# Kernel tuning notes

Measured on AMD Instinct MI355X. Metric: run time of the kernel, lower is better.

## Reference

```python
import jax, jax.numpy as jnp
import numpy as np
from jax import lax

B, N_PATCH, D_ENC, D, L, HEADS, NCLS = 2, 640, 512, 256, 2, 8, 3
IMG, PS, NSC = 256, 16, 2
MAX_SCALE = NSC - 1
NEW_GS = IMG // (PS // (2 ** MAX_SCALE))  # 32
STAGES = 3  # log2(IMG / NEW_GS)
HD = D // HEADS


def _make_patch_code():
    # valid multiscale partition, sorted by scale (the torch code assumes this)
    base = IMG // PS  # 16x16 scale-0 grid
    pc = []
    for c in range(base * base // 2):
        pc.append((0, c))
    for c in range(base * base // 2, base * base):
        r0, c0 = divmod(c, base)
        for a in range(2):
            for b in range(2):
                pc.append((1, (2 * r0 + a) * (2 * base) + (2 * c0 + b)))
    return np.asarray(pc, dtype=np.int64)


def setup_inputs():
    key = jax.random.key(0)
    ks = iter(jax.random.split(key, 48))
    nrm = lambda *s: jax.random.normal(next(ks), s, jnp.float32) * 0.02
    z = lambda *s: jnp.zeros(s, jnp.float32)
    o = lambda *s: jnp.ones(s, jnp.float32)
    return {
        "x": jax.random.normal(next(ks), (B, N_PATCH, D_ENC), jnp.float32),
        "patch_code": jnp.asarray(_make_patch_code()),
        "proj_dec_w": nrm(D_ENC, D), "proj_dec_b": z(D),
        "pos_w1": nrm(2, D), "pos_b1": z(D),
        "pos_w2": nrm(D, D), "pos_b2": z(D),
        "cls_emb": nrm(1, D, D),
        "ln1_g": o(L, D), "ln1_b": z(L, D),
        "qkv_w": nrm(L, D, 3 * D), "qkv_b": z(L, 3 * D),
        "attn_w": nrm(L, D, D), "attn_b": z(L, D),
        "ln2_g": o(L, D), "ln2_b": z(L, D),
        "mlp_w1": nrm(L, D, 4 * D), "mlp_b1": z(L, 4 * D),
        "mlp_w2": nrm(L, 4 * D, D), "mlp_b2": z(L, D),
        "dec_g": o(D), "dec_b": z(D),
        "proj_patch": jax.random.normal(next(ks), (D, D), jnp.float32) * D ** -0.5,
        "proj_classes": jax.random.normal(next(ks), (D, D), jnp.float32) * D ** -0.5,
        "mask_g": o(D), "mask_b": z(D),
        "up_conv_w": nrm(STAGES, D, D, 3, 3), "up_conv_b": z(STAGES, D),
        "up_convt_w": nrm(STAGES, D, D, 2, 2), "up_convt_b": z(STAGES, D),
        "out_conv_w": nrm(NCLS, D, 3, 3), "out_conv_b": z(NCLS),
    }


def _ln(x, g, b, eps=1e-5):
    m = x.mean(-1, keepdims=True)
    v = jnp.mean((x - m) ** 2, axis=-1, keepdims=True)
    return (x - m) / jnp.sqrt(v + eps) * g + b


def _inorm(x, eps=1e-5):  # InstanceNorm2d, affine=False
    m = x.mean((2, 3), keepdims=True)
    v = jnp.mean((x - m) ** 2, axis=(2, 3), keepdims=True)
    return (x - m) / jnp.sqrt(v + eps)


def _leaky(x):
    return jnp.where(x >= 0, x, 0.01 * x)


def _conv3(x, w, b):
    y = lax.conv_general_dilated(x, w, (1, 1), 'SAME', dimension_numbers=('NCHW', 'OIHW', 'NCHW'))
    return y + b[None, :, None, None]


def _convt2(x, w, b):
    # ConvTranspose2d(k=2, s=2): non-overlapping, exact as einsum + reshape
    bsz, _, h, wd = x.shape
    y = jnp.einsum('bchw,cdij->bdhiwj', x, w).reshape(bsz, w.shape[1], 2 * h, 2 * wd)
    return y + b[None, :, None, None]


def _block(x, l, ln1_g, ln1_b, qkv_w, qkv_b, attn_w, attn_b, ln2_g, ln2_b, mlp_w1, mlp_b1, mlp_w2, mlp_b2):
    bsz, s, _ = x.shape
    h = _ln(x, ln1_g[l], ln1_b[l])
    qkv = (h @ qkv_w[l] + qkv_b[l]).reshape(bsz, s, 3, HEADS, HD)
    q, k, v = qkv[:, :, 0], qkv[:, :, 1], qkv[:, :, 2]  # [b,s,h,d]
    att = jax.nn.softmax(jnp.einsum('bqhd,bkhd->bhqk', q, k) * HD ** -0.5, axis=-1)
    out = jnp.einsum('bhqk,bkhd->bqhd', att, v).reshape(bsz, s, D)
    x = x + out @ attn_w[l] + attn_b[l]
    h = _ln(x, ln2_g[l], ln2_b[l])
    x = x + jax.nn.gelu(h @ mlp_w1[l] + mlp_b1[l], approximate=False) @ mlp_w2[l] + mlp_b2[l]
    return x


def reference(x, patch_code, proj_dec_w, proj_dec_b, pos_w1, pos_b1, pos_w2, pos_b2, cls_emb, ln1_g, ln1_b, qkv_w, qkv_b, attn_w, attn_b, ln2_g, ln2_b, mlp_w1, mlp_b1, mlp_w2, mlp_b2, dec_g, dec_b, proj_patch, proj_classes, mask_g, mask_b, up_conv_w, up_conv_b, up_convt_w, up_convt_b, out_conv_w, out_conv_b):
    bsz = x.shape[0]
    x = x @ proj_dec_w + proj_dec_b
    pcf = patch_code.astype(jnp.float32)
    pos = jax.nn.relu(pcf @ pos_w1 + pos_b1) @ pos_w2 + pos_b2  # [N, D]
    x = x + pos[None]
    x = jnp.concatenate([x, jnp.broadcast_to(cls_emb, (bsz, D, D))], axis=1)  # seq = N + D
    for l in range(L):
        x = _block(x, l, ln1_g, ln1_b, qkv_w, qkv_b, attn_w, attn_b, ln2_g, ln2_b, mlp_w1, mlp_b1, mlp_w2, mlp_b2)
    x = _ln(x, dec_g, dec_b)
    patches, cls_feat = x[:, :-D], x[:, -D:]
    patches = patches @ proj_patch
    cls_feat = cls_feat @ proj_classes
    patches = patches / jnp.linalg.norm(patches, axis=-1, keepdims=True)
    cls_feat = cls_feat / jnp.linalg.norm(cls_feat, axis=-1, keepdims=True)
    masks = _ln(jnp.einsum('bnd,bkd->bnk', patches, cls_feat), mask_g, mask_b)  # [B,N,D]
    vals = masks.transpose(0, 2, 1)  # [B, C=D, N]
    # patches_to_images: scatter variable-size patches into the finest grid.
    # Implemented as an inverse map (cell -> source patch) + gather, which is
    # exact because patch_code is a partition of the image.
    s = patch_code[:, 0]
    coord = patch_code[:, 1]
    gs = (IMG // PS) * jnp.power(2, s)          # grid size at each patch's scale
    k = jnp.power(2, MAX_SCALE - s)             # footprint in finest-grid cells
    r = (coord // gs) * k
    c = (coord % gs) * k
    K = 2 ** MAX_SCALE
    oi = jnp.arange(K)[:, None]
    oj = jnp.arange(K)[None, :]
    rr = r[:, None, None] + oi[None]
    cc = c[:, None, None] + oj[None]
    valid = (oi[None] < k[:, None, None]) & (oj[None] < k[:, None, None])
    flat = jnp.where(valid, rr * NEW_GS + cc, NEW_GS * NEW_GS).reshape(-1)
    pid = jnp.broadcast_to(jnp.arange(N_PATCH)[:, None, None], (N_PATCH, K, K)).reshape(-1)
    inv = jnp.zeros(NEW_GS * NEW_GS + 1, jnp.int32).at[flat].set(pid.astype(jnp.int32))
    img = vals[:, :, inv[:NEW_GS * NEW_GS]].reshape(bsz, D, NEW_GS, NEW_GS)
    for i in range(STAGES):
        img = _leaky(_inorm(_conv3(img, up_conv_w[i], up_conv_b[i])))
        img = _leaky(_inorm(_convt2(img, up_convt_w[i], up_convt_b[i])))
    return _conv3(img, out_conv_w, out_conv_b)  # [B, n_cls, 256, 256]
```

## Files before the change

### kernel.cpp

```cpp
#include <hip/hip_runtime.h>
#include <hip/hip_bf16.h>

typedef __hip_bfloat16 bf16;
typedef _Float16 f16;
typedef __attribute__((ext_vector_type(8))) _Float16 f16x8;
typedef __attribute__((ext_vector_type(4))) float f32x4;

__global__ void detect_k(const unsigned short* __restrict__ xh, int* __restrict__ flags)
{
  const int t = threadIdx.x;
  int w = 0;
  for (int i = t; i < 512; i += 64) {
    const int e = (xh[i] >> 7) & 0xFF;
    if (e == 0xFF || e >= 0x88) ++w;
  }
  #pragma unroll
  for (int msk = 1; msk < 64; msk <<= 1) w += __shfl_xor(w, msk);
  if (t == 0) flags[0] = (w > 32) ? 1 : 0;
}

#define NSEG 33
struct CvtDesc {
  const void* src[NSEG];
  unsigned dstOff[NSEG];
  unsigned n[NSEG];
};
__global__ __launch_bounds__(256) void cvtall_k(
    CvtDesc d, float* __restrict__ P, const int* __restrict__ flags)
{
  const int s = blockIdx.y;
  const unsigned n = d.n[s];
  const int fp32 = flags[0];
  float* dst = P + d.dstOff[s];
  const unsigned stride = gridDim.x * 256u;
  if (fp32) {
    const float* src = (const float*)d.src[s];
    for (unsigned i = blockIdx.x * 256u + threadIdx.x; i < n; i += stride) dst[i] = src[i];
  } else {
    const bf16* src = (const bf16*)d.src[s];
    for (unsigned i = blockIdx.x * 256u + threadIdx.x; i < n; i += stride)
      dst[i] = __bfloat162float(src[i]);
  }
}

__global__ __launch_bounds__(256) void prepw_k(
    const float* __restrict__ ucw, const float* __restrict__ utw, const float* __restrict__ ocw,
    f16* __restrict__ wf3, f16* __restrict__ wt, f16* __restrict__ wocp)
{
  const int n1 = 3 * 9 * 65536;
  const int n2 = 3 * 4 * 65536;
  const int n3 = 9 * 16 * 256;
  for (int i = blockIdx.x * 256 + threadIdx.x; i < n1 + n2 + n3; i += gridDim.x * 256) {
    if (i < n1) {
      const int st = i / 589824, r = i % 589824;
      const int kk = r / 65536, rr = r % 65536;
      const int co = rr >> 8, ci = rr & 255;
      wf3[i] = (f16)ucw[(((size_t)st * 256 + co) * 256 + ci) * 9 + kk];
    } else if (i < n1 + n2) {
      const int j = i - n1;
      const int st = j / 262144, r = j % 262144;
      const int ij = r / 65536, rr = r % 65536;
      const int co = rr >> 8, ci = rr & 255;
      wt[j] = (f16)utw[(((size_t)st * 256 + ci) * 256 + co) * 4 + ij];
    } else {
      const int j = i - n1 - n2;
      const int tap = j >> 12, rem = j & 4095;
      const int co = rem >> 8, ci = rem & 255;
      wocp[j] = (co < 3) ? (f16)ocw[(((size_t)co * 256) + ci) * 9 + tap] : (f16)0.f;
    }
  }
}

template<bool TRB, int ACT>
__global__ __launch_bounds__(256) void gemm64_k(
    const float* __restrict__ A, const float* __restrict__ B,
    const float* __restrict__ bias, const float* __restrict__ res,
    float* __restrict__ C, int M, int N, int K)
{
  const int m0 = blockIdx.y << 6, n0 = blockIdx.x << 6;
  const int t = threadIdx.x;
  const int lane = t & 63, wv = t >> 6;
  const int wm = wv >> 1, wn = wv & 1;
  const int frow = lane & 15, kg = lane >> 4;
  __shared__ f16 As[64][40];
  __shared__ f16 Bs[64][40];
  f32x4 acc[2][2];
  #pragma unroll
  for (int i = 0; i < 2; ++i)
    #pragma unroll
    for (int j = 0; j < 2; ++j) acc[i][j] = (f32x4){0.f, 0.f, 0.f, 0.f};

  for (int k0 = 0; k0 < K; k0 += 32) {
    __syncthreads();
    {
      const int row = t >> 2, kh = (t & 3) << 3;
      const float* ap = A + (size_t)(m0 + row) * K + k0 + kh;
      #pragma unroll
      for (int j = 0; j < 8; ++j) As[row][kh + j] = (f16)ap[j];
    }
    if (TRB) {
      const int row = t >> 2, kh = (t & 3) << 3;
      const float* bp = B + (size_t)(n0 + row) * K + k0 + kh;
      #pragma unroll
      for (int j = 0; j < 8; ++j) Bs[row][kh + j] = (f16)bp[j];
    } else {
      #pragma unroll
      for (int i2 = 0; i2 < 8; ++i2) {
        const int i = i2 * 256 + t;
        const int n = i & 63, kk = i >> 6;
        Bs[n][kk] = (f16)B[(size_t)(k0 + kk) * N + n0 + n];
      }
    }
    __syncthreads();
    f16x8 af[2], bf[2];
    #pragma unroll
    for (int fm = 0; fm < 2; ++fm)
      af[fm] = *(const f16x8*)&As[wm * 32 + fm * 16 + frow][kg * 8];
    #pragma unroll
    for (int fn = 0; fn < 2; ++fn)
      bf[fn] = *(const f16x8*)&Bs[wn * 32 + fn * 16 + frow][kg * 8];
    #pragma unroll
    for (int fm = 0; fm < 2; ++fm)
      #pragma unroll
      for (int fn = 0; fn < 2; ++fn)
        acc[fm][fn] = __builtin_amdgcn_mfma_f32_16x16x32_f16(af[fm], bf[fn], acc[fm][fn], 0, 0, 0);
  }
  #pragma unroll
  for (int fn = 0; fn < 2; ++fn) {
    const int col = n0 + wn * 32 + fn * 16 + frow;
    const float bv = bias ? bias[col] : 0.f;
    #pragma unroll
    for (int fm = 0; fm < 2; ++fm)
      #pragma unroll
      for (int r = 0; r < 4; ++r) {
        const int row = m0 + wm * 32 + fm * 16 + kg * 4 + r;
        float v = acc[fm][fn][r] + bv;
        if (ACT == 1) v = 0.5f * v * (1.0f + erff(v * 0.70710678118654752f));
        if (res) v += res[(size_t)row * N + col];
        C[(size_t)row * N + col] = v;
      }
  }
}

__global__ __launch_bounds__(256) void ln_k(
    const float* __restrict__ in, float* __restrict__ out,
    const float* __restrict__ g, const float* __restrict__ b)
{
  const int row = blockIdx.x, t = threadIdx.x;
  __shared__ float ws1[4], ws2[4];
  const float x = in[(size_t)row * 256 + t];
  float v = x;
  #pragma unroll
  for (int msk = 1; msk < 64; msk <<= 1) v += __shfl_xor(v, msk);
  if ((t & 63) == 0) ws1[t >> 6] = v;
  __syncthreads();
  const float m = (ws1[0] + ws1[1] + ws1[2] + ws1[3]) * (1.0f / 256.0f);
  const float d = x - m;
  float v2 = d * d;
  #pragma unroll
  for (int msk = 1; msk < 64; msk <<= 1) v2 += __shfl_xor(v2, msk);
  if ((t & 63) == 0) ws2[t >> 6] = v2;
  __syncthreads();
  const float rstd = rsqrtf((ws2[0] + ws2[1] + ws2[2] + ws2[3]) * (1.0f / 256.0f) + 1e-5f);
  out[(size_t)row * 256 + t] = d * rstd * g[t] + b[t];
}

__global__ __launch_bounds__(256) void l2n_k(float* __restrict__ x)
{
  const int row = blockIdx.x, t = threadIdx.x;
  __shared__ float ws[4];
  const float v = x[(size_t)row * 256 + t];
  float s = v * v;
  #pragma unroll
  for (int msk = 1; msk < 64; msk <<= 1) s += __shfl_xor(s, msk);
  if ((t & 63) == 0) ws[t >> 6] = s;
  __syncthreads();
  x[(size_t)row * 256 + t] = v * rsqrtf(ws[0] + ws[1] + ws[2] + ws[3]);
}

__global__ __launch_bounds__(256) void posh_k(
    const int* __restrict__ pc, const float* __restrict__ w1, const float* __restrict__ b1,
    float* __restrict__ hid)
{
  const int n = blockIdx.x, t = threadIdx.x;
  const int wide = (pc[3] == 0);
  const int sv = wide ? pc[4 * n] : pc[2 * n];
  const int cv = wide ? pc[4 * n + 2] : pc[2 * n + 1];
  const float hv = (float)sv * w1[t] + (float)cv * w1[256 + t] + b1[t];
  hid[(size_t)n * 256 + t] = hv > 0.0f ? hv : 0.0f;
}

__global__ __launch_bounds__(256) void assemble_k(
    const float* __restrict__ proj, const float* __restrict__ pos,
    const float* __restrict__ cls, float* __restrict__ xb)
{
  const int row = blockIdx.x;
  const int b = row / 896, n = row % 896, t = threadIdx.x;
  float v;
  if (n < 640) v = proj[((size_t)b * 640 + n) * 256 + t] + pos[n * 256 + t];
  else         v = cls[(n - 640) * 256 + t];
  xb[(size_t)row * 256 + t] = v;
}

__global__ __launch_bounds__(128) void attnm_k(
    const float* __restrict__ qkv, float* __restrict__ out)
{
  const int q0 = blockIdx.x << 5;
  const int h = blockIdx.y, b = blockIdx.z;
  const int t = threadIdx.x;
  const int lane = t & 63, wv = t >> 6;
  const int c = lane & 15, kg = lane >> 4;
  __shared__ f16 Qs[32][36];
  __shared__ f16 Ks[64][36];
  __shared__ f16 Vt[32][68];
  __shared__ f16 Pl[2][16][68];
  {
    const int row = t >> 2, part = t & 3;
    const float* src = qkv + ((size_t)(b * 896 + q0 + row) * 768) + h * 32 + part * 8;
    f16 tmp[8];
    #pragma unroll
    for (int j = 0; j < 8; ++j) tmp[j] = (f16)(src[j] * 0.17677669529663687f);
    *(f16x8*)&Qs[row][part * 8] = *(const f16x8*)tmp;
  }
  const f32x4 z4 = {0.f, 0.f, 0.f, 0.f};
  f32x4 o0 = z4, o1 = z4;
  float m[4] = {-1e30f, -1e30f, -1e30f, -1e30f};
  float l[4] = {0.f, 0.f, 0.f, 0.f};

  for (int k0 = 0; k0 < 896; k0 += 64) {
    __syncthreads();
    for (int i = t; i < 256; i += 128) {
      const int row = i >> 2, part = i & 3;
      const float* src = qkv + ((size_t)(b * 896 + k0 + row) * 768) + 256 + h * 32 + part * 8;
      f16 tmp[8];
      #pragma unroll
      for (int j = 0; j < 8; ++j) tmp[j] = (f16)src[j];
      *(f16x8*)&Ks[row][part * 8] = *(const f16x8*)tmp;
    }
    for (int i = t; i < 256; i += 128) {
      const int row = i >> 2, part = i & 3;
      const float* src = qkv + ((size_t)(b * 896 + k0 + row) * 768) + 512 + h * 32 + part * 8;
      #pragma unroll
      for (int j = 0; j < 8; ++j) Vt[part * 8 + j][row] = (f16)src[j];
    }
    __syncthreads();
    const f16x8 aq = *(const f16x8*)&Qs[wv * 16 + c][kg * 8];
    f32x4 s[4];
    #pragma unroll
    for (int fn = 0; fn < 4; ++fn)
      s[fn] = __builtin_amdgcn_mfma_f32_16x16x32_f16(
          aq, *(const f16x8*)&Ks[fn * 16 + c][kg * 8], z4, 0, 0, 0);
    float sc[4];
    #pragma unroll
    for (int r = 0; r < 4; ++r) {
      float v = fmaxf(fmaxf(s[0][r], s[1][r]), fmaxf(s[2][r], s[3][r]));
      #pragma unroll
      for (int msk = 1; msk < 16; msk <<= 1) v = fmaxf(v, __shfl_xor(v, msk));
      const float mn = fmaxf(m[r], v);
      sc[r] = __expf(m[r] - mn);
      m[r] = mn;
    }
    #pragma unroll
    for (int r = 0; r < 4; ++r) {
      float ps = 0.f;
      #pragma unroll
      for (int fn = 0; fn < 4; ++fn) {
        const float p = __expf(s[fn][r] - m[r]);
        ps += p;
        Pl[wv][kg * 4 + r][fn * 16 + c] = (f16)p;
      }
      #pragma unroll
      for (int msk = 1; msk < 16; msk <<= 1) ps += __shfl_xor(ps, msk);
      l[r] = l[r] * sc[r] + ps;
    }
    #pragma unroll
    for (int r = 0; r < 4; ++r) { o0[r] *= sc[r]; o1[r] *= sc[r]; }
    const f16x8 a0 = *(const f16x8*)&Pl[wv][c][kg * 8];
    const f16x8 a1 = *(const f16x8*)&Pl[wv][c][32 + kg * 8];
    o0 = __builtin_amdgcn_mfma_f32_16x16x32_f16(a0, *(const f16x8*)&Vt[c][kg * 8], o0, 0, 0, 0);
    o0 = __builtin_amdgcn_mfma_f32_16x16x32_f16(a1, *(const f16x8*)&Vt[c][32 + kg * 8], o0, 0, 0, 0);
    o1 = __builtin_amdgcn_mfma_f32_16x16x32_f16(a0, *(const f16x8*)&Vt[16 + c][kg * 8], o1, 0, 0, 0);
    o1 = __builtin_amdgcn_mfma_f32_16x16x32_f16(a1, *(const f16x8*)&Vt[16 + c][32 + kg * 8], o1, 0, 0, 0);
  }
  #pragma unroll
  for (int r = 0; r < 4; ++r) {
    const int row = q0 + wv * 16 + kg * 4 + r;
    const float inv = 1.0f / l[r];
    out[((size_t)(b * 896 + row) * 256) + h * 32 + c] = o0[r] * inv;
    out[((size_t)(b * 896 + row) * 256) + h * 32 + 16 + c] = o1[r] * inv;
  }
}

__global__ __launch_bounds__(1024) void inv_k(const int* __restrict__ pc, int* __restrict__ inv)
{
  const int t = threadIdx.x;
  if (t < 1024) inv[t] = 0;
  __syncthreads();
  if (t < 640) {
    const int wide = (pc[3] == 0);
    int s = wide ? pc[4 * t] : pc[2 * t];
    int coord = wide ? pc[4 * t + 2] : pc[2 * t + 1];
    s &= 1;
    const int gs = 16 << s;
    const int k = 1 << (1 - s);
    const int r = (coord / gs) * k, c = (coord % gs) * k;
    for (int oi = 0; oi < k; ++oi)
      for (int oj = 0; oj < k; ++oj) {
        const int rr = r + oi, cc = c + oj;
        if (rr >= 0 && rr < 32 && cc >= 0 && cc < 32)
          inv[rr * 32 + cc] = t;
      }
  }
}

__global__ __launch_bounds__(256) void gather16_k(
    const float* __restrict__ masks, const int* __restrict__ inv, f16* __restrict__ img)
{
  const int p = blockIdx.x & 1023, b = blockIdx.x >> 10, t = threadIdx.x;
  img[((size_t)blockIdx.x << 8) + t] = (f16)masks[((size_t)b * 640 + inv[p]) * 256 + t];
}

__global__ __launch_bounds__(256) void conv3m_k(
    const f16* __restrict__ x, const f16* __restrict__ wf, const float* __restrict__ bias,
    f16* __restrict__ y, int H, int W)
{
  const int tilesx = W >> 4;
  const int ty0 = (blockIdx.x / tilesx) << 4, tx0 = (blockIdx.x % tilesx) << 4;
  const int co0 = blockIdx.y << 6;
  const int b = blockIdx.z;
  const int t = threadIdx.x;
  const int lane = t & 63, wv = t >> 6;
  const int frow = lane & 15, kg = lane >> 4;
  __shared__ f16 halo[18][18][40];
  __shared__ f16 bt9[9][64][40];
  f32x4 acc[4][4];
  #pragma unroll
  for (int i = 0; i < 4; ++i)
    #pragma unroll
    for (int j = 0; j < 4; ++j) acc[i][j] = (f32x4){0.f, 0.f, 0.f, 0.f};

  for (int c0 = 0; c0 < 256; c0 += 32) {
    __syncthreads();
    for (int i = t; i < 1296; i += 256) {
      const int cell = i >> 2, part = i & 3;
      const int hy = cell / 18, hx = cell - hy * 18;
      const int gy = ty0 + hy - 1, gx = tx0 + hx - 1;
      f16x8 v = {(f16)0,(f16)0,(f16)0,(f16)0,(f16)0,(f16)0,(f16)0,(f16)0};
      if (gy >= 0 && gy < H && gx >= 0 && gx < W)
        v = *(const f16x8*)&x[(((size_t)b * H + gy) * W + gx) * 256 + c0 + part * 8];
      *(f16x8*)&halo[hy][hx][part * 8] = v;
    }
    for (int i = t; i < 2304; i += 256) {
      const int tap = i >> 8, rem = i & 255, co = rem >> 2, part = rem & 3;
      *(f16x8*)&bt9[tap][co][part * 8] =
          *(const f16x8*)&wf[(((size_t)tap * 256) + co0 + co) * 256 + c0 + part * 8];
    }
    __syncthreads();
    #pragma unroll
    for (int kyr = 0; kyr < 3; ++kyr)
      #pragma unroll
      for (int kx = 0; kx < 3; ++kx) {
        f16x8 af[4], bf[4];
        #pragma unroll
        for (int fm = 0; fm < 4; ++fm) {
          const int pos = wv * 64 + fm * 16 + frow;
          af[fm] = *(const f16x8*)&halo[(pos >> 4) + kyr][(pos & 15) + kx][kg * 8];
        }
        #pragma unroll
        for (int fn = 0; fn < 4; ++fn)
          bf[fn] = *(const f16x8*)&bt9[kyr * 3 + kx][fn * 16 + frow][kg * 8];
        #pragma unroll
        for (int fm = 0; fm < 4; ++fm)
          #pragma unroll
          for (int fn = 0; fn < 4; ++fn)
            acc[fm][fn] = __builtin_amdgcn_mfma_f32_16x16x32_f16(af[fm], bf[fn], acc[fm][fn], 0, 0, 0);
      }
  }
  #pragma unroll
  for (int fn = 0; fn < 4; ++fn) {
    const int col = co0 + fn * 16 + frow;
    const float bv = bias[col];
    #pragma unroll
    for (int fm = 0; fm < 4; ++fm)
      #pragma unroll
      for (int r = 0; r < 4; ++r) {
        const int pos = wv * 64 + fm * 16 + kg * 4 + r;
        y[(((size_t)b * H + ty0 + (pos >> 4)) * W + tx0 + (pos & 15)) * 256 + col] =
            (f16)(acc[fm][fn][r] + bv);
      }
  }
}

__global__ __launch_bounds__(256) void convtm_k(
    const f16* __restrict__ x, const f16* __restrict__ wtp, const float* __restrict__ bias,
    f16* __restrict__ y, int H, int W)
{
  const int tilesx = W >> 4;
  const int ty0 = (blockIdx.x / tilesx) << 4, tx0 = (blockIdx.x % tilesx) << 4;
  const int co0 = (blockIdx.y >> 2) << 6;
  const int par = blockIdx.y & 3;
  const int pa = par >> 1, pb = par & 1;
  const int b = blockIdx.z;
  const int t = threadIdx.x;
  const int lane = t & 63, wv = t >> 6;
  const int frow = lane & 15, kg = lane >> 4;
  __shared__ f16 at[256][40];
  __shared__ f16 btw[64][40];
  f32x4 acc[4][4];
  #pragma unroll
  for (int i = 0; i < 4; ++i)
    #pragma unroll
    for (int j = 0; j < 4; ++j) acc[i][j] = (f32x4){0.f, 0.f, 0.f, 0.f};

  for (int c0 = 0; c0 < 256; c0 += 32) {
    __syncthreads();
    for (int i = t; i < 1024; i += 256) {
      const int cell = i >> 2, part = i & 3;
      const int gy = ty0 + (cell >> 4), gx = tx0 + (cell & 15);
      *(f16x8*)&at[cell][part * 8] =
          *(const f16x8*)&x[(((size_t)b * H + gy) * W + gx) * 256 + c0 + part * 8];
    }
    {
      const int i = t;
      const int co = i >> 2, part = i & 3;
      *(f16x8*)&btw[co][part * 8] =
          *(const f16x8*)&wtp[((size_t)par * 256 + co0 + co) * 256 + c0 + part * 8];
    }
    __syncthreads();
    f16x8 af[4], bf[4];
    #pragma unroll
    for (int fm = 0; fm < 4; ++fm)
      af[fm] = *(const f16x8*)&at[wv * 64 + fm * 16 + frow][kg * 8];
    #pragma unroll
    for (int fn = 0; fn < 4; ++fn)
      bf[fn] = *(const f16x8*)&btw[fn * 16 + frow][kg * 8];
    #pragma unroll
    for (int fm = 0; fm < 4; ++fm)
      #pragma unroll
      for (int fn = 0; fn < 4; ++fn)
        acc[fm][fn] = __builtin_amdgcn_mfma_f32_16x16x32_f16(af[fm], bf[fn], acc[fm][fn], 0, 0, 0);
  }
  const int HO = H << 1, WO = W << 1;
  #pragma unroll
  for (int fn = 0; fn < 4; ++fn) {
    const int col = co0 + fn * 16 + frow;
    const float bv = bias[col];
    #pragma unroll
    for (int fm = 0; fm < 4; ++fm)
      #pragma unroll
      for (int r = 0; r < 4; ++r) {
        const int pos = wv * 64 + fm * 16 + kg * 4 + r;
        const int oy = ((ty0 + (pos >> 4)) << 1) + pa;
        const int ox = ((tx0 + (pos & 15)) << 1) + pb;
        y[(((size_t)b * HO + oy) * WO + ox) * 256 + col] = (f16)(acc[fm][fn][r] + bv);
      }
  }
}

__global__ __launch_bounds__(256) void stats1v_k(
    const f16* __restrict__ x, float2* __restrict__ partial, int HW, int NS)
{
  const int s = blockIdx.x, b = blockIdx.y, t = threadIdx.x;
  const int rg = t >> 5, cp = t & 31;
  const int rpb = HW / NS;
  const f16* p = x + ((size_t)b * HW + (size_t)s * rpb) * 256 + cp * 8;
  float s1[8] = {}, s2[8] = {};
  for (int r = rg; r < rpb; r += 8) {
    const f16x8 v = *(const f16x8*)&p[(size_t)r * 256];
    #pragma unroll
    for (int j = 0; j < 8; ++j) { const float f = (float)v[j]; s1[j] += f; s2[j] += f * f; }
  }
  __shared__ float red[2][8][256];
  #pragma unroll
  for (int j = 0; j < 8; ++j) { red[0][rg][cp * 8 + j] = s1[j]; red[1][rg][cp * 8 + j] = s2[j]; }
  __syncthreads();
  float a1 = 0.f, a2 = 0.f;
  #pragma unroll
  for (int g = 0; g < 8; ++g) { a1 += red[0][g][t]; a2 += red[1][g][t]; }
  partial[((size_t)b * NS + s) * 256 + t] = make_float2(a1, a2);
}

__global__ __launch_bounds__(256) void stats2_k(
    const float2* __restrict__ partial, float2* __restrict__ mr, int HW)
{
  const int cg = blockIdx.x, b = blockIdx.y, t = threadIdx.x;
  const int chl = t & 31, g = t >> 5;
  const int ch = cg * 32 + chl;
  float s1 = 0.f, s2 = 0.f;
  for (int s = g * 16; s < g * 16 + 16; ++s) {
    const float2 v = partial[((size_t)b * 128 + s) * 256 + ch];
    s1 += v.x; s2 += v.y;
  }
  __shared__ float r1[8][32], r2[8][32];
  r1[g][chl] = s1; r2[g][chl] = s2;
  __syncthreads();
  if (t < 32) {
    float a1 = 0.f, a2 = 0.f;
    #pragma unroll
    for (int gg = 0; gg < 8; ++gg) { a1 += r1[gg][t]; a2 += r2[gg][t]; }
    const float m = a1 / (float)HW;
    const float var = fmaxf(a2 / (float)HW - m * m, 0.f);
    mr[b * 256 + cg * 32 + t] = make_float2(m, rsqrtf(var + 1e-5f));
  }
}

__global__ __launch_bounds__(256) void norm8_k(
    f16* __restrict__ x, const float2* __restrict__ mr, int HW)
{
  const int b = blockIdx.y, t = threadIdx.x;
  const int cp = t & 31, rg = t >> 5;
  float2 mv[8];
  {
    const float2* mrb = mr + b * 256 + cp * 8;
    #pragma unroll
    for (int j = 0; j < 8; ++j) mv[j] = mrb[j];
  }
  f16* p = x + ((size_t)b * HW + (size_t)blockIdx.x * 64) * 256 + cp * 8;
  #pragma unroll
  for (int r8 = 0; r8 < 8; ++r8) {
    const int r = rg + r8 * 8;
    f16x8 v = *(const f16x8*)&p[(size_t)r * 256];
    #pragma unroll
    for (int j = 0; j < 8; ++j) {
      const float z = ((float)v[j] - mv[j].x) * mv[j].y;
      v[j] = (f16)(z >= 0.f ? z : 0.01f * z);
    }
    *(f16x8*)&p[(size_t)r * 256] = v;
  }
}

__global__ __launch_bounds__(256) void convoutm2_k(
    const f16* __restrict__ x, const f16* __restrict__ wocp, const float* __restrict__ bias,
    void* __restrict__ yv, const int* __restrict__ flags)
{
  const int ty0 = (blockIdx.x >> 4) << 4, tx0 = (blockIdx.x & 15) << 4;
  const int b = blockIdx.y;
  const int t = threadIdx.x;
  const int lane = t & 63, wv = t >> 6;
  const int frow = lane & 15, kg = lane >> 4;
  __shared__ f16 halo[18][18][40];
  f32x4 acc[4];
  #pragma unroll
  for (int i = 0; i < 4; ++i) acc[i] = (f32x4){0.f, 0.f, 0.f, 0.f};

  for (int c0 = 0; c0 < 256; c0 += 32) {
    __syncthreads();
    for (int i = t; i < 1296; i += 256) {
      const int cell = i >> 2, part = i & 3;
      const int hy = cell / 18, hx = cell - hy * 18;
      const int gy = ty0 + hy - 1, gx = tx0 + hx - 1;
      f16x8 v = {(f16)0,(f16)0,(f16)0,(f16)0,(f16)0,(f16)0,(f16)0,(f16)0};
      if ((unsigned)gy < 256u && (unsigned)gx < 256u)
        v = *(const f16x8*)&x[(((size_t)b * 256 + gy) * 256 + gx) * 256 + c0 + part * 8];
      *(f16x8*)&halo[hy][hx][part * 8] = v;
    }
    __syncthreads();
    #pragma unroll
    for (int kyr = 0; kyr < 3; ++kyr)
      #pragma unroll
      for (int kx = 0; kx < 3; ++kx) {
        const int tap = kyr * 3 + kx;
        const f16x8 bf = *(const f16x8*)&wocp[((size_t)(tap * 16 + frow)) * 256 + c0 + kg * 8];
        #pragma unroll
        for (int fm = 0; fm < 4; ++fm) {
          const int pos = wv * 64 + fm * 16 + frow;
          const f16x8 af = *(const f16x8*)&halo[(pos >> 4) + kyr][(pos & 15) + kx][kg * 8];
          acc[fm] = __builtin_amdgcn_mfma_f32_16x16x32_f16(af, bf, acc[fm], 0, 0, 0);
        }
      }
  }
  if (frow < 3) {
    const int fp32 = flags[0];
    const float bv = bias[frow];
    #pragma unroll
    for (int fm = 0; fm < 4; ++fm)
      #pragma unroll
      for (int r = 0; r < 4; ++r) {
        const int pos = wv * 64 + fm * 16 + kg * 4 + r;
        const int oy = ty0 + (pos >> 4), ox = tx0 + (pos & 15);
        const size_t oidx = (((size_t)b * 3 + frow) * 256 + oy) * 256 + ox;
        const float v = acc[fm][r] + bv;
        if (fp32) ((float*)yv)[oidx] = v;
        else      ((bf16*)yv)[oidx] = __float2bfloat16(v);
      }
  }
}

extern "C" void kernel_launch(void* const* d_in, const int* in_sizes, int n_in,
                              void* d_out, int out_size, void* d_ws, size_t ws_size,
                              hipStream_t stream) {
  (void)in_sizes; (void)n_in; (void)out_size; (void)ws_size;
  const int* pc = (const int*)d_in[1];

  float* P = (float*)d_ws;
  size_t off = 0;
  CvtDesc cd{};
  int seg = 0;
  auto alloc = [&](size_t n) { float* p = P + off; off += n; return p; };
  auto allocCv = [&](int idx, size_t n) {
    float* p = P + off;
    cd.src[seg] = d_in[idx]; cd.dstOff[seg] = (unsigned)off; cd.n[seg] = (unsigned)n;
    ++seg; off += n; return p;
  };

  int*    flags   = (int*)alloc(16);
  int*    invbuf  = (int*)alloc(1024);
  float2* partial = (float2*)alloc(131072);
  float2* mr1     = (float2*)alloc(1024);
  float* pdb   = allocCv(3, 256);
  float* pw1   = allocCv(4, 512);
  float* pb1   = allocCv(5, 256);
  float* pb2   = allocCv(7, 256);
  float* pln1g = allocCv(9, 512);
  float* pln1b = allocCv(10, 512);
  float* pqkvb = allocCv(12, 1536);
  float* pattb = allocCv(14, 512);
  float* pln2g = allocCv(15, 512);
  float* pln2b = allocCv(16, 512);
  float* pm1b  = allocCv(18, 2048);
  float* pm2b  = allocCv(20, 512);
  float* pdecg = allocCv(21, 256);
  float* pdecb = allocCv(22, 256);
  float* pmg   = allocCv(25, 256);
  float* pmb   = allocCv(26, 256);
  float* pucb  = allocCv(28, 768);
  float* putb  = allocCv(30, 768);
  float* pocw  = allocCv(31, 6912);
  float* pocb  = allocCv(32, 16);
  off = (off + 255) & ~(size_t)255;
  f16* wf3  = (f16*)alloc(884736);
  f16* wt   = (f16*)alloc(393216);
  f16* wocp = (f16*)alloc(18432);
  off = (off + 255) & ~(size_t)255;

  float* zoneA = P + off;
  f16*   R2h   = (f16*)zoneA;
  {
    size_t zo = off;
    auto zCv = [&](int idx, size_t n) {
      float* p = P + zo;
      cd.src[seg] = d_in[idx]; cd.dstOff[seg] = (unsigned)zo; cd.n[seg] = (unsigned)n;
      ++seg; zo += n; return p;
    };
    float* px    = zCv(0, 655360);
    float* pdw   = zCv(2, 131072);
    float* pw2   = zCv(6, 65536);
    float* pcls  = zCv(8, 65536);
    float* pqkvw = zCv(11, 393216);
    float* pattw = zCv(13, 131072);
    float* pm1w  = zCv(17, 524288);
    float* pm2w  = zCv(19, 524288);
    float* pprp  = zCv(23, 65536);
    float* pprc  = zCv(24, 65536);
    float* pucw  = zCv(27, 1769472);
    float* putw  = zCv(29, 786432);
    float* xbuf   = P + zo; zo += 458752;
    float* hbuf   = P + zo; zo += 458752;
    float* qkvbuf = P + zo; zo += 1376256;
    float* hidbuf = P + zo; zo += 1835008;
    float* posbuf = P + zo; zo += 163840;
    float* patbuf = P + zo; zo += 327680;
    float* clsbuf = P + zo; zo += 131072;
    float* masksb = P + zo; zo += 327680;
    off += 16777216;
    f16* R0h = (f16*)(P + off); off += 4194304;
    f16* R1h = (f16*)(P + off); off += 4194304;

    detect_k<<<1, 64, 0, stream>>>((const unsigned short*)d_in[0], flags);
    cvtall_k<<<dim3(256, NSEG), 256, 0, stream>>>(cd, P, flags);
    prepw_k<<<2048, 256, 0, stream>>>(pucw, putw, pocw, wf3, wt, wocp);

    posh_k<<<640, 256, 0, stream>>>(pc, pw1, pb1, patbuf);
    gemm64_k<false, 0><<<dim3(4, 10), 256, 0, stream>>>(
        patbuf, pw2, pb2, nullptr, posbuf, 640, 256, 256);
    gemm64_k<false, 0><<<dim3(4, 20), 256, 0, stream>>>(
        px, pdw, pdb, nullptr, hidbuf, 1280, 256, 512);
    assemble_k<<<1792, 256, 0, stream>>>(hidbuf, posbuf, pcls, xbuf);

    for (int l = 0; l < 2; ++l) {
      ln_k<<<1792, 256, 0, stream>>>(xbuf, hbuf, pln1g + l * 256, pln1b + l * 256);
      gemm64_k<false, 0><<<dim3(12, 28), 256, 0, stream>>>(
          hbuf, pqkvw + (size_t)l * 196608, pqkvb + l * 768, nullptr, qkvbuf, 1792, 768, 256);
      attnm_k<<<dim3(28, 8, 2), 128, 0, stream>>>(qkvbuf, hbuf);
      gemm64_k<false, 0><<<dim3(4, 28), 256, 0, stream>>>(
          hbuf, pattw + (size_t)l * 65536, pattb + l * 256, xbuf, xbuf, 1792, 256, 256);
      ln_k<<<1792, 256, 0, stream>>>(xbuf, hbuf, pln2g + l * 256, pln2b + l * 256);
      gemm64_k<false, 1><<<dim3(16, 28), 256, 0, stream>>>(
          hbuf, pm1w + (size_t)l * 262144, pm1b + l * 1024, nullptr, hidbuf, 1792, 1024, 256);
      gemm64_k<false, 0><<<dim3(4, 28), 256, 0, stream>>>(
          hidbuf, pm2w + (size_t)l * 262144, pm2b + l * 256, xbuf, xbuf, 1792, 256, 1024);
    }

    ln_k<<<1792, 256, 0, stream>>>(xbuf, hbuf, pdecg, pdecb);
    for (int b = 0; b < 2; ++b) {
      gemm64_k<false, 0><<<dim3(4, 10), 256, 0, stream>>>(
          hbuf + (size_t)b * 896 * 256, pprp, nullptr, nullptr,
          patbuf + (size_t)b * 640 * 256, 640, 256, 256);
      gemm64_k<false, 0><<<dim3(4, 4), 256, 0, stream>>>(
          hbuf + ((size_t)b * 896 + 640) * 256, pprc, nullptr, nullptr,
          clsbuf + (size_t)b * 65536, 256, 256, 256);
    }
    l2n_k<<<1280, 256, 0, stream>>>(patbuf);
    l2n_k<<<512, 256, 0, stream>>>(clsbuf);
    for (int b = 0; b < 2; ++b) {
      gemm64_k<true, 0><<<dim3(4, 10), 256, 0, stream>>>(
          patbuf + (size_t)b * 163840, clsbuf + (size_t)b * 65536, nullptr, nullptr,
          masksb + (size_t)b * 163840, 640, 256, 256);
    }
    ln_k<<<1280, 256, 0, stream>>>(masksb, masksb, pmg, pmb);

    inv_k<<<1, 1024, 0, stream>>>(pc, invbuf);
    gather16_k<<<2048, 256, 0, stream>>>(masksb, invbuf, R0h);

    int H = 32;
    for (int i = 0; i < 3; ++i) {
      conv3m_k<<<dim3((H / 16) * (H / 16), 4, 2), 256, 0, stream>>>(
          R0h, wf3 + (size_t)i * 9 * 65536, pucb + i * 256, R1h, H, H);
      const int hw1 = H * H;
      stats1v_k<<<dim3(128, 2), 256, 0, stream>>>(R1h, partial, hw1, 128);
      stats2_k<<<dim3(8, 2), 256, 0, stream>>>(partial, mr1, hw1);
      norm8_k<<<dim3(hw1 / 64, 2), 256, 0, stream>>>(R1h, mr1, hw1);
      f16* dst = (i == 2) ? R2h : R0h;
      convtm_k<<<dim3((H / 16) * (H / 16), 16, 2), 256, 0, stream>>>(
          R1h, wt + (size_t)i * 4 * 65536, putb + i * 256, dst, H, H);
      const int hw2 = 4 * H * H;
      stats1v_k<<<dim3(128, 2), 256, 0, stream>>>(dst, partial, hw2, 128);
      stats2_k<<<dim3(8, 2), 256, 0, stream>>>(partial, mr1, hw2);
      norm8_k<<<dim3(hw2 / 64, 2), 256, 0, stream>>>(dst, mr1, hw2);
      H *= 2;
    }

    convoutm2_k<<<dim3(256, 2), 256, 0, stream>>>(R2h, wocp, pocb, d_out, flags);
  }
}
```

Before: 675.8 us.

## Fuse instance-norm stats into conv epilogues and normalization into next conv loads

Conv and transposed-conv kernels now accumulate per-channel sum and sum-of-squares in their epilogue, writing per-tile partials, removing the separate stats pass over the activation. The normalize+leaky-ReLU step is applied on the fly when the following conv (or the output conv) loads its input tiles, removing the separate in-place normalization pass. This removes several full-tensor read/write passes per stage at the cost of redundant normalization of halo elements and extra epilogue reductions.

```diff
diff --git a/kernel.cpp b/kernel.cpp
--- a/kernel.cpp
+++ b/kernel.cpp
@@ -320,19 +320,33 @@
   img[((size_t)blockIdx.x << 8) + t] = (f16)masks[((size_t)b * 640 + inv[p]) * 256 + t];
 }
 
+__device__ __forceinline__ f16x8 nrm8(f16x8 v, const float2* __restrict__ mrb, int cbase)
+{
+  #pragma unroll
+  for (int j = 0; j < 8; ++j) {
+    const float2 mv = mrb[cbase + j];
+    float z = ((float)v[j] - mv.x) * mv.y;
+    v[j] = (f16)(z >= 0.f ? z : 0.01f * z);
+  }
+  return v;
+}
+
+template<bool NORM>
 __global__ __launch_bounds__(256) void conv3m_k(
     const f16* __restrict__ x, const f16* __restrict__ wf, const float* __restrict__ bias,
-    f16* __restrict__ y, int H, int W)
+    f16* __restrict__ y, int H, int W, const float2* __restrict__ mr, float2* __restrict__ partial)
 {
   const int tilesx = W >> 4;
   const int ty0 = (blockIdx.x / tilesx) << 4, tx0 = (blockIdx.x % tilesx) << 4;
   const int co0 = blockIdx.y << 6;
-  const int b = blockIdx.z;
+  const int bb = blockIdx.z;
   const int t = threadIdx.x;
   const int lane = t & 63, wv = t >> 6;
   const int frow = lane & 15, kg = lane >> 4;
+  const float2* mrb = NORM ? mr + bb * 256 : nullptr;
   __shared__ f16 halo[18][18][40];
   __shared__ f16 bt9[9][64][40];
+  __shared__ float2 sred[4][64];
   f32x4 acc[4][4];
   #pragma unroll
   for (int i = 0; i < 4; ++i)
@@ -346,8 +360,10 @@
       const int hy = cell / 18, hx = cell - hy * 18;
       const int gy = ty0 + hy - 1, gx = tx0 + hx - 1;
       f16x8 v = {(f16)0,(f16)0,(f16)0,(f16)0,(f16)0,(f16)0,(f16)0,(f16)0};
-      if (gy >= 0 && gy < H && gx >= 0 && gx < W)
-        v = *(const f16x8*)&x[(((size_t)b * H + gy) * W + gx) * 256 + c0 + part * 8];
+      if (gy >= 0 && gy < H && gx >= 0 && gx < W) {
+        v = *(const f16x8*)&x[(((size_t)bb * H + gy) * W + gx) * 256 + c0 + part * 8];
+        if (NORM) v = nrm8(v, mrb, c0 + part * 8);
+      }
       *(f16x8*)&halo[hy][hx][part * 8] = v;
     }
     for (int i = t; i < 2304; i += 256) {
@@ -376,6 +392,7 @@
             acc[fm][fn] = __builtin_amdgcn_mfma_f32_16x16x32_f16(af[fm], bf[fn], acc[fm][fn], 0, 0, 0);
       }
   }
+  float ps[4] = {0.f, 0.f, 0.f, 0.f}, ss[4] = {0.f, 0.f, 0.f, 0.f};
   #pragma unroll
   for (int fn = 0; fn < 4; ++fn) {
     const int col = co0 + fn * 16 + frow;
@@ -385,27 +402,49 @@
       #pragma unroll
       for (int r = 0; r < 4; ++r) {
         const int pos = wv * 64 + fm * 16 + kg * 4 + r;
-        y[(((size_t)b * H + ty0 + (pos >> 4)) * W + tx0 + (pos & 15)) * 256 + col] =
-            (f16)(acc[fm][fn][r] + bv);
-      }
+        const float v = acc[fm][fn][r] + bv;
+        ps[fn] += v; ss[fn] += v * v;
+        y[(((size_t)bb * H + ty0 + (pos >> 4)) * W + tx0 + (pos & 15)) * 256 + col] = (f16)v;
+      }
+  }
+  #pragma unroll
+  for (int fn = 0; fn < 4; ++fn)
+    #pragma unroll
+    for (int msk = 16; msk < 64; msk <<= 1) {
+      ps[fn] += __shfl_xor(ps[fn], msk);
+      ss[fn] += __shfl_xor(ss[fn], msk);
+    }
+  __syncthreads();
+  if (kg == 0) {
+    #pragma unroll
+    for (int fn = 0; fn < 4; ++fn) sred[wv][fn * 16 + frow] = make_float2(ps[fn], ss[fn]);
+  }
+  __syncthreads();
+  if (t < 64) {
+    float a1 = 0.f, a2 = 0.f;
+    #pragma unroll
+    for (int w = 0; w < 4; ++w) { a1 += sred[w][t].x; a2 += sred[w][t].y; }
+    partial[((size_t)bb * 256 + blockIdx.x) * 256 + co0 + t] = make_float2(a1, a2);
   }
 }
 
 __global__ __launch_bounds__(256) void convtm_k(
     const f16* __restrict__ x, const f16* __restrict__ wtp, const float* __restrict__ bias,
-    f16* __restrict__ y, int H, int W)
+    f16* __restrict__ y, int H, int W, const float2* __restrict__ mr, float2* __restrict__ partial)
 {
   const int tilesx = W >> 4;
   const int ty0 = (blockIdx.x / tilesx) << 4, tx0 = (blockIdx.x % tilesx) << 4;
   const int co0 = (blockIdx.y >> 2) << 6;
   const int par = blockIdx.y & 3;
   const int pa = par >> 1, pb = par & 1;
-  const int b = blockIdx.z;
+  const int bb = blockIdx.z;
   const int t = threadIdx.x;
   const int lane = t & 63, wv = t >> 6;
   const int frow = lane & 15, kg = lane >> 4;
+  const float2* mrb = mr + bb * 256;
   __shared__ f16 at[256][40];
   __shared__ f16 btw[64][40];
+  __shared__ float2 sred[4][64];
   f32x4 acc[4][4];
   #pragma unroll
   for (int i = 0; i < 4; ++i)
@@ -417,8 +456,8 @@
     for (int i = t; i < 1024; i += 256) {
       const int cell = i >> 2, part = i & 3;
       const int gy = ty0 + (cell >> 4), gx = tx0 + (cell & 15);
-      *(f16x8*)&at[cell][part * 8] =
-          *(const f16x8*)&x[(((size_t)b * H + gy) * W + gx) * 256 + c0 + part * 8];
+      f16x8 v = *(const f16x8*)&x[(((size_t)bb * H + gy) * W + gx) * 256 + c0 + part * 8];
+      *(f16x8*)&at[cell][part * 8] = nrm8(v, mrb, c0 + part * 8);
     }
     {
       const int i = t;
@@ -441,6 +480,7 @@
         acc[fm][fn] = __builtin_amdgcn_mfma_f32_16x16x32_f16(af[fm], bf[fn], acc[fm][fn], 0, 0, 0);
   }
   const int HO = H << 1, WO = W << 1;
+  float ps[4] = {0.f, 0.f, 0.f, 0.f}, ss[4] = {0.f, 0.f, 0.f, 0.f};
   #pragma unroll
   for (int fn = 0; fn < 4; ++fn) {
     const int col = co0 + fn * 16 + frow;
@@ -452,43 +492,41 @@
         const int pos = wv * 64 + fm * 16 + kg * 4 + r;
         const int oy = ((ty0 + (pos >> 4)) << 1) + pa;
         const int ox = ((tx0 + (pos & 15)) << 1) + pb;
-        y[(((size_t)b * HO + oy) * WO + ox) * 256 + col] = (f16)(acc[fm][fn][r] + bv);
-      }
-  }
-}
-
-__global__ __launch_bounds__(256) void stats1v_k(
-    const f16* __restrict__ x, float2* __restrict__ partial, int HW, int NS)
-{
-  const int s = blockIdx.x, b = blockIdx.y, t = threadIdx.x;
-  const int rg = t >> 5, cp = t & 31;
-  const int rpb = HW / NS;
-  const f16* p = x + ((size_t)b * HW + (size_t)s * rpb) * 256 + cp * 8;
-  float s1[8] = {}, s2[8] = {};
-  for (int r = rg; r < rpb; r += 8) {
-    const f16x8 v = *(const f16x8*)&p[(size_t)r * 256];
-    #pragma unroll
-    for (int j = 0; j < 8; ++j) { const float f = (float)v[j]; s1[j] += f; s2[j] += f * f; }
-  }
-  __shared__ float red[2][8][256];
-  #pragma unroll
-  for (int j = 0; j < 8; ++j) { red[0][rg][cp * 8 + j] = s1[j]; red[1][rg][cp * 8 + j] = s2[j]; }
-  __syncthreads();
-  float a1 = 0.f, a2 = 0.f;
-  #pragma unroll
-  for (int g = 0; g < 8; ++g) { a1 += red[0][g][t]; a2 += red[1][g][t]; }
-  partial[((size_t)b * NS + s) * 256 + t] = make_float2(a1, a2);
-}
-
-__global__ __launch_bounds__(256) void stats2_k(
-    const float2* __restrict__ partial, float2* __restrict__ mr, int HW)
+        const float v = acc[fm][fn][r] + bv;
+        ps[fn] += v; ss[fn] += v * v;
+        y[(((size_t)bb * HO + oy) * WO + ox) * 256 + col] = (f16)v;
+      }
+  }
+  #pragma unroll
+  for (int fn = 0; fn < 4; ++fn)
+    #pragma unroll
+    for (int msk = 16; msk < 64; msk <<= 1) {
+      ps[fn] += __shfl_xor(ps[fn], msk);
+      ss[fn] += __shfl_xor(ss[fn], msk);
+    }
+  __syncthreads();
+  if (kg == 0) {
+    #pragma unroll
+    for (int fn = 0; fn < 4; ++fn) sred[wv][fn * 16 + frow] = make_float2(ps[fn], ss[fn]);
+  }
+  __syncthreads();
+  if (t < 64) {
+    float a1 = 0.f, a2 = 0.f;
+    #pragma unroll
+    for (int w = 0; w < 4; ++w) { a1 += sred[w][t].x; a2 += sred[w][t].y; }
+    partial[((size_t)bb * 256 + blockIdx.x * 4 + par) * 256 + co0 + t] = make_float2(a1, a2);
+  }
+}
+
+__global__ __launch_bounds__(256) void stats2v2_k(
+    const float2* __restrict__ partial, float2* __restrict__ mr, int HW, int NS)
 {
   const int cg = blockIdx.x, b = blockIdx.y, t = threadIdx.x;
   const int chl = t & 31, g = t >> 5;
   const int ch = cg * 32 + chl;
   float s1 = 0.f, s2 = 0.f;
-  for (int s = g * 16; s < g * 16 + 16; ++s) {
-    const float2 v = partial[((size_t)b * 128 + s) * 256 + ch];
+  for (int s = g; s < NS; s += 8) {
+    const float2 v = partial[((size_t)b * 256 + s) * 256 + ch];
     s1 += v.x; s2 += v.y;
   }
   __shared__ float r1[8][32], r2[8][32];
@@ -504,40 +542,16 @@
   }
 }
 
-__global__ __launch_bounds__(256) void norm8_k(
-    f16* __restrict__ x, const float2* __restrict__ mr, int HW)
-{
-  const int b = blockIdx.y, t = threadIdx.x;
-  const int cp = t & 31, rg = t >> 5;
-  float2 mv[8];
-  {
-    const float2* mrb = mr + b * 256 + cp * 8;
-    #pragma unroll
-    for (int j = 0; j < 8; ++j) mv[j] = mrb[j];
-  }
-  f16* p = x + ((size_t)b * HW + (size_t)blockIdx.x * 64) * 256 + cp * 8;
-  #pragma unroll
-  for (int r8 = 0; r8 < 8; ++r8) {
-    const int r = rg + r8 * 8;
-    f16x8 v = *(const f16x8*)&p[(size_t)r * 256];
-    #pragma unroll
-    for (int j = 0; j < 8; ++j) {
-      const float z = ((float)v[j] - mv[j].x) * mv[j].y;
-      v[j] = (f16)(z >= 0.f ? z : 0.01f * z);
-    }
-    *(f16x8*)&p[(size_t)r * 256] = v;
-  }
-}
-
 __global__ __launch_bounds__(256) void convoutm2_k(
     const f16* __restrict__ x, const f16* __restrict__ wocp, const float* __restrict__ bias,
-    void* __restrict__ yv, const int* __restrict__ flags)
+    void* __restrict__ yv, const int* __restrict__ flags, const float2* __restrict__ mr)
 {
   const int ty0 = (blockIdx.x >> 4) << 4, tx0 = (blockIdx.x & 15) << 4;
   const int b = blockIdx.y;
   const int t = threadIdx.x;
   const int lane = t & 63, wv = t >> 6;
   const int frow = lane & 15, kg = lane >> 4;
+  const float2* mrb = mr + b * 256;
   __shared__ f16 halo[18][18][40];
   f32x4 acc[4];
   #pragma unroll
@@ -550,8 +564,10 @@
       const int hy = cell / 18, hx = cell - hy * 18;
       const int gy = ty0 + hy - 1, gx = tx0 + hx - 1;
       f16x8 v = {(f16)0,(f16)0,(f16)0,(f16)0,(f16)0,(f16)0,(f16)0,(f16)0};
-      if ((unsigned)gy < 256u && (unsigned)gx < 256u)
+      if ((unsigned)gy < 256u && (unsigned)gx < 256u) {
         v = *(const f16x8*)&x[(((size_t)b * 256 + gy) * 256 + gx) * 256 + c0 + part * 8];
+        v = nrm8(v, mrb, c0 + part * 8);
+      }
       *(f16x8*)&halo[hy][hx][part * 8] = v;
     }
     __syncthreads();
@@ -605,7 +621,7 @@
 
   int*    flags   = (int*)alloc(16);
   int*    invbuf  = (int*)alloc(1024);
-  float2* partial = (float2*)alloc(131072);
+  float2* partial = (float2*)alloc(262144);
   float2* mr1     = (float2*)alloc(1024);
   float* pdb   = allocCv(3, 256);
   float* pw1   = allocCv(4, 512);
@@ -714,22 +730,21 @@
 
     int H = 32;
     for (int i = 0; i < 3; ++i) {
-      conv3m_k<<<dim3((H / 16) * (H / 16), 4, 2), 256, 0, stream>>>(
-          R0h, wf3 + (size_t)i * 9 * 65536, pucb + i * 256, R1h, H, H);
-      const int hw1 = H * H;
-      stats1v_k<<<dim3(128, 2), 256, 0, stream>>>(R1h, partial, hw1, 128);
-      stats2_k<<<dim3(8, 2), 256, 0, stream>>>(partial, mr1, hw1);
-      norm8_k<<<dim3(hw1 / 64, 2), 256, 0, stream>>>(R1h, mr1, hw1);
+      const int tiles = (H / 16) * (H / 16);
+      if (i == 0)
+        conv3m_k<false><<<dim3(tiles, 4, 2), 256, 0, stream>>>(
+            R0h, wf3, pucb, R1h, H, H, nullptr, partial);
+      else
+        conv3m_k<true><<<dim3(tiles, 4, 2), 256, 0, stream>>>(
+            R0h, wf3 + (size_t)i * 9 * 65536, pucb + i * 256, R1h, H, H, mr1, partial);
+      stats2v2_k<<<dim3(8, 2), 256, 0, stream>>>(partial, mr1, H * H, tiles);
       f16* dst = (i == 2) ? R2h : R0h;
-      convtm_k<<<dim3((H / 16) * (H / 16), 16, 2), 256, 0, stream>>>(
-          R1h, wt + (size_t)i * 4 * 65536, putb + i * 256, dst, H, H);
-      const int hw2 = 4 * H * H;
-      stats1v_k<<<dim3(128, 2), 256, 0, stream>>>(dst, partial, hw2, 128);
-      stats2_k<<<dim3(8, 2), 256, 0, stream>>>(partial, mr1, hw2);
-      norm8_k<<<dim3(hw2 / 64, 2), 256, 0, stream>>>(dst, mr1, hw2);
+      convtm_k<<<dim3(tiles, 16, 2), 256, 0, stream>>>(
+          R1h, wt + (size_t)i * 4 * 65536, putb + i * 256, dst, H, H, mr1, partial);
+      stats2v2_k<<<dim3(8, 2), 256, 0, stream>>>(partial, mr1, 4 * H * H, tiles * 4);
       H *= 2;
     }
 
-    convoutm2_k<<<dim3(256, 2), 256, 0, stream>>>(R2h, wocp, pocb, d_out, flags);
-  }
-}
+    convoutm2_k<<<dim3(256, 2), 256, 0, stream>>>(R2h, wocp, pocb, d_out, flags, mr1);
+  }
+}
```

After: 691.0 us. 1.02x slower.
